# Performance work log

Hardware: AMD Instinct MI355X
Metric: run time of the kernel (lower is better)

The kernel has to match this reference:

```python
import jax, jax.numpy as jnp
import numpy as np

N_NODES = 100000
N_EDGES = 1600000
IN_DIM, HID_DIM, OUT_DIM = 128, 128, 64


def setup_inputs() -> dict:
    key = jax.random.key(0)
    ks = jax.random.split(key, 5)
    x = jax.random.normal(ks[0], (N_NODES, IN_DIM), dtype=jnp.float32)
    edge_index = jax.random.randint(ks[1], (2, N_EDGES), 0, N_NODES, dtype=jnp.int64)
    W1 = jax.random.normal(ks[2], (IN_DIM, HID_DIM), dtype=jnp.float32) * (1.0 / np.sqrt(IN_DIM))
    b1 = jnp.zeros((HID_DIM,), dtype=jnp.float32)
    W2 = jax.random.normal(ks[3], (HID_DIM, OUT_DIM), dtype=jnp.float32) * (1.0 / np.sqrt(HID_DIM))
    b2 = jnp.zeros((OUT_DIM,), dtype=jnp.float32)
    return {"x": x, "edge_index": edge_index, "W1": W1, "b1": b1, "W2": W2, "b2": b2}


def _gcn_conv(h, row, col, norm, b, n_nodes):
    # h: [N, F] already linearly transformed; message = norm_e * h[src]; scatter-add to dst
    msg = h[row] * norm[:, None]                      # [E+N, F]
    out = jax.ops.segment_sum(msg, col, num_segments=n_nodes)
    return out + b


def reference(x, edge_index, W1, b1, W2, b2):
    n = x.shape[0]
    loops = jnp.arange(n, dtype=edge_index.dtype)
    row = jnp.concatenate([edge_index[0], loops])     # sources (incl. self loops)
    col = jnp.concatenate([edge_index[1], loops])     # targets
    # symmetric normalization: deg over targets with unit edge weights
    deg = jax.ops.segment_sum(jnp.ones_like(col, dtype=x.dtype), col, num_segments=n)
    dinv = jnp.where(deg > 0, jax.lax.rsqrt(jnp.maximum(deg, 1.0)), 0.0)
    norm = dinv[row] * dinv[col]                      # [E+N]
    h = jax.nn.relu(_gcn_conv(x @ W1, row, col, norm, b1, n))
    out = _gcn_conv(h @ W2, row, col, norm, b2, n)
    return out.mean(axis=0)                           # [OUT_DIM]
```

## Files before the change

### kernel.cpp

```cpp
#include <hip/hip_runtime.h>

#define N_NODES 100000
#define N_EDGES 1600000
#define IN_DIM 128
#define HID_DIM 128
#define OUT_DIM 64
#define BKT_SHIFT 7
#define BKT_SIZE 128
#define NBKT ((N_NODES + BKT_SIZE - 1) / BKT_SIZE)
#define B1 256
#define HIST_N (NBKT * B1)
#define HIST_N2 (2 * HIST_N)
#define GEMM_BLKS ((N_NODES + 127) / 128)
#define AGG_BLKS 2048
#define NPW 13

typedef float v2f __attribute__((ext_vector_type(2)));
typedef float v4f __attribute__((ext_vector_type(4)));
typedef short v8s __attribute__((ext_vector_type(8)));

__device__ __forceinline__ int permb(int b) { return ((b & 7) << 5) | (b >> 3); }

__device__ __forceinline__ unsigned int f2bf(float f) {
  unsigned int u = __float_as_uint(f);
  return (u + 0x7FFFu + ((u >> 16) & 1u)) >> 16;
}

template <bool HI>
__device__ __forceinline__ v2f cvt8(unsigned int u) {
  return __builtin_amdgcn_cvt_pk_f32_fp8((int)u, HI);
}

__device__ __forceinline__ float redq(float v) {
  v += __shfl_xor(v, 16);
  v += __shfl_xor(v, 32);
  return v;
}

__device__ __forceinline__ void load4(const void* ei, int is64, int half, int base,
                                      int* v) {
  if (is64) {
    const long long* e = (const long long*)ei + (size_t)half * N_EDGES + base;
    longlong2 a = *(const longlong2*)e;
    longlong2 b = *(const longlong2*)(e + 2);
    v[0] = (int)a.x; v[1] = (int)a.y; v[2] = (int)b.x; v[3] = (int)b.y;
  } else {
    const int* e = (const int*)ei + (size_t)half * N_EDGES + base;
    int4 a = *(const int4*)e;
    v[0] = a.x; v[1] = a.y; v[2] = a.z; v[3] = a.w;
  }
}

__device__ __forceinline__ int detect64_block(const unsigned int* ei, int* sh) {
  if (threadIdx.x == 0) *sh = 0;
  __syncthreads();
  if (ei[1 + 2 * threadIdx.x] != 0u) *sh = 1;
  __syncthreads();
  return (*sh == 0) ? 1 : 0;
}

__global__ __launch_bounds__(256) void front_kernel(const float* __restrict__ x,
                                                    const float* __restrict__ W,
                                                    const void* ei,
                                                    unsigned int* __restrict__ G,
                                                    int* hist, float* S) {
  __shared__ __align__(16) char smem[2 * 128 * 136 * 2];
  if (blockIdx.x >= GEMM_BLKS) {
    int* hd = (int*)smem;
    int* hs = hd + NBKT;
    int* sh = hs + NBKT;
    const int hb = blockIdx.x - GEMM_BLKS;
    const int pj = permb(hb);
    if (hb == 0 && threadIdx.x < HID_DIM) S[threadIdx.x] = 0.f;
    const int is64 = detect64_block((const unsigned int*)ei, sh);
    for (int k = threadIdx.x; k < NBKT; k += 256) { hd[k] = 0; hs[k] = 0; }
    __syncthreads();
    for (int g = hb * 256 + threadIdx.x; g < N_EDGES / 4; g += B1 * 256) {
      int r[4], c[4];
      load4(ei, is64, 0, g * 4, r);
      load4(ei, is64, 1, g * 4, c);
#pragma unroll
      for (int k = 0; k < 4; k++) {
        atomicAdd(&hd[c[k] >> BKT_SHIFT], 1);
        atomicAdd(&hs[r[k] >> BKT_SHIFT], 1);
      }
    }
    __syncthreads();
    for (int k = threadIdx.x; k < NBKT; k += 256) {
      hist[k * B1 + pj] = hd[k];
      hist[HIST_N + k * B1 + pj] = hs[k];
    }
    return;
  }
  typedef unsigned short us_row[136];
  us_row* lx = (us_row*)smem;
  us_row* lwt = (us_row*)(smem + 128 * 136 * 2);
  const int t = threadIdx.x;
  const int row0 = blockIdx.x * 128;

  {
    const float4* W4 = (const float4*)W;
    for (int it = 0; it < 16; ++it) {
      int idx = t + 256 * it;
      int k = idx >> 5, c4 = (idx & 31) * 4;
      float4 w = W4[idx];
      lwt[c4 + 0][k] = (unsigned short)f2bf(w.x);
      lwt[c4 + 1][k] = (unsigned short)f2bf(w.y);
      lwt[c4 + 2][k] = (unsigned short)f2bf(w.z);
      lwt[c4 + 3][k] = (unsigned short)f2bf(w.w);
    }
  }
  {
    const float4* x4 = (const float4*)(x + (size_t)row0 * IN_DIM);
    for (int it = 0; it < 16; ++it) {
      int idx = t + 256 * it;
      int r = idx >> 5, kq = (idx & 31) * 4;
      float4 v = make_float4(0.f, 0.f, 0.f, 0.f);
      if (row0 + r < N_NODES) v = x4[idx];
      unsigned int p0 = (f2bf(v.y) << 16) | f2bf(v.x);
      unsigned int p1 = (f2bf(v.w) << 16) | f2bf(v.z);
      *(uint2*)&lx[r][kq] = make_uint2(p0, p1);
    }
  }
  __syncthreads();

  const int lane = t & 63;
  const int wv = t >> 6;
  const int m0 = wv * 32;
  const int lrow = lane & 15;
  const int lk = (lane >> 4) * 8;

  v4f acc[2][8];
#pragma unroll
  for (int si = 0; si < 2; si++)
#pragma unroll
    for (int n = 0; n < 8; n++) acc[si][n] = (v4f){0.f, 0.f, 0.f, 0.f};

#pragma unroll
  for (int kk = 0; kk < 128; kk += 32) {
    v8s a0 = *(const v8s*)&lx[m0 + lrow][kk + lk];
    v8s a1 = *(const v8s*)&lx[m0 + 16 + lrow][kk + lk];
#pragma unroll
    for (int n = 0; n < 8; n++) {
      v8s b = *(const v8s*)&lwt[n * 16 + lrow][kk + lk];
      acc[0][n] = __builtin_amdgcn_mfma_f32_16x16x32_bf16(a0, b, acc[0][n], 0, 0, 0);
      acc[1][n] = __builtin_amdgcn_mfma_f32_16x16x32_bf16(a1, b, acc[1][n], 0, 0, 0);
    }
  }

  unsigned char* G8 = (unsigned char*)G;
#pragma unroll
  for (int si = 0; si < 2; si++)
#pragma unroll
    for (int n = 0; n < 8; n++) {
      int colg = n * 16 + (lane & 15);
#pragma unroll
      for (int i = 0; i < 4; i++) {
        int r = row0 + m0 + si * 16 + (lane >> 4) * 4 + i;
        if (r < N_NODES) {
          float v = acc[si][n][i];
          int pk = __builtin_amdgcn_cvt_pk_fp8_f32(v, v, 0, false);
          G8[(size_t)r * HID_DIM + colg] = (unsigned char)(pk & 0xFF);
        }
      }
    }
}

__global__ void scan1_kernel(int* arr, int* bsum, int n) {
  __shared__ int tmp[256];
  int i = blockIdx.x * 256 + threadIdx.x;
  int v = (i < n) ? arr[i] : 0;
  tmp[threadIdx.x] = v;
  __syncthreads();
  for (int off = 1; off < 256; off <<= 1) {
    int t2 = (threadIdx.x >= off) ? tmp[threadIdx.x - off] : 0;
    __syncthreads();
    tmp[threadIdx.x] += t2;
    __syncthreads();
  }
  if (i < n) arr[i] = tmp[threadIdx.x] - v;
  if (threadIdx.x == 255) bsum[blockIdx.x] = tmp[255];
}

__global__ void scan2_kernel(int* bsum, int nb) {
  __shared__ int tmp[1024];
  const int t = threadIdx.x;
  int v0 = (2 * t < nb) ? bsum[2 * t] : 0;
  int v1 = (2 * t + 1 < nb) ? bsum[2 * t + 1] : 0;
  int s = v0 + v1;
  tmp[t] = s;
  __syncthreads();
  for (int off = 1; off < 1024; off <<= 1) {
    int t2 = (t >= off) ? tmp[t - off] : 0;
    __syncthreads();
    tmp[t] += t2;
    __syncthreads();
  }
  int excl = tmp[t] - s;
  if (2 * t < nb) bsum[2 * t] = excl;
  if (2 * t + 1 < nb) bsum[2 * t + 1] = excl + v0;
}

__global__ __launch_bounds__(256) void scatter_kernel(const void* ei, const int* hist,
                                                      const int* bsum,
                                                      unsigned int* pairs) {
  __shared__ int cd[NBKT], cs[NBKT], sh[1];
  const int is64 = detect64_block((const unsigned int*)ei, sh);
  const int pj = permb(blockIdx.x);
  for (int k = threadIdx.x; k < NBKT; k += 256) {
    cd[k] = hist[k * B1 + pj] + bsum[k];
    cs[k] = hist[HIST_N + k * B1 + pj] + bsum[NBKT + k];
  }
  __syncthreads();
  for (int g = blockIdx.x * 256 + threadIdx.x; g < N_EDGES / 4; g += B1 * 256) {
    int r[4], c[4];
    load4(ei, is64, 0, g * 4, r);
    load4(ei, is64, 1, g * 4, c);
#pragma unroll
    for (int k = 0; k < 4; k++) {
      int pd = atomicAdd(&cd[c[k] >> BKT_SHIFT], 1);
      pairs[pd] = ((unsigned int)(c[k] & (BKT_SIZE - 1)) << 17) | (unsigned int)r[k];
      int ps = atomicAdd(&cs[r[k] >> BKT_SHIFT], 1);
      pairs[ps] = ((unsigned int)(r[k] & (BKT_SIZE - 1)) << 17) | (unsigned int)c[k];
    }
  }
}

__global__ __launch_bounds__(256) void csrA_kernel(const int* hist, const int* bsum,
                                                   const unsigned int* pairs,
                                                   int* rowptr, float* dinv) {
  __shared__ int cnt[BKT_SIZE], sc[BKT_SIZE];
  const int k = blockIdx.x;
  const int base = hist[k * B1] + bsum[k];
  const int end = (k == NBKT - 1) ? N_EDGES : hist[(k + 1) * B1] + bsum[k + 1];
  const int nseg = end - base;
  const int l = threadIdx.x;
  if (l < BKT_SIZE) cnt[l] = 0;
  __syncthreads();
  for (int i = l; i < nseg; i += 256) atomicAdd(&cnt[pairs[base + i] >> 17], 1);
  __syncthreads();
  if (l < BKT_SIZE) sc[l] = cnt[l];
  __syncthreads();
  for (int off = 1; off < BKT_SIZE; off <<= 1) {
    int v = (l < BKT_SIZE && l >= off) ? sc[l - off] : 0;
    __syncthreads();
    if (l < BKT_SIZE) sc[l] += v;
    __syncthreads();
  }
  if (l < BKT_SIZE) {
    int excl = sc[l] - cnt[l];
    int v = k * BKT_SIZE + l;
    if (v < N_NODES) {
      rowptr[v] = base + excl;
      dinv[v] = rsqrtf((float)(cnt[l] + 1));
    }
  }
  if (k == NBKT - 1 && l == 0) rowptr[N_NODES] = N_EDGES;
}

__global__ __launch_bounds__(256) void csrBout_kernel(const int* hist, const int* bsum,
                                                      const unsigned int* pairs,
                                                      const int* __restrict__ rowptr,
                                                      const float* __restrict__ dinv,
                                                      unsigned int* __restrict__ csr,
                                                      float* __restrict__ wacc) {
  if (blockIdx.x < NBKT) {
    __shared__ int cur[BKT_SIZE];
    const int k = blockIdx.x;
    const int base = hist[k * B1] + bsum[k];
    const int end = (k == NBKT - 1) ? N_EDGES : hist[(k + 1) * B1] + bsum[k + 1];
    const int nseg = end - base;
    const int l = threadIdx.x;
    if (l < BKT_SIZE) {
      int v = k * BKT_SIZE + l;
      cur[l] = (v < N_NODES) ? rowptr[v] : 0;
    }
    __syncthreads();
    for (int i = l; i < nseg; i += 256) {
      unsigned int pk = pairs[base + i];
      unsigned int src = pk & 0x1FFFFu;
      int pos = atomicAdd(&cur[pk >> 17], 1);
      unsigned int bits = f2bf(dinv[src]);
      csr[pos] = (bits << 17) | src;
    }
    return;
  }
  __shared__ float fb[BKT_SIZE];
  const int k = blockIdx.x - NBKT;
  const int base = hist[HIST_N + k * B1] + bsum[NBKT + k];
  const int end =
      (k == NBKT - 1) ? 2 * N_EDGES : hist[HIST_N + (k + 1) * B1] + bsum[NBKT + k + 1];
  if (threadIdx.x < BKT_SIZE) fb[threadIdx.x] = 0.f;
  __syncthreads();
  for (int i = base + threadIdx.x; i < end; i += 256) {
    unsigned int pk = pairs[i];
    atomicAdd(&fb[pk >> 17], dinv[pk & 0x1FFFFu]);
  }
  __syncthreads();
  int v = k * BKT_SIZE + threadIdx.x;
  if (threadIdx.x < BKT_SIZE && v < N_NODES) wacc[v] = fb[threadIdx.x];
}

__global__ __launch_bounds__(256) void aggregate_kernel(
    const unsigned int* __restrict__ G, const int* __restrict__ rowptr,
    const unsigned int* __restrict__ csr, const float* __restrict__ dinv,
    const float* __restrict__ wacc, const float* __restrict__ b1,
    float* __restrict__ S) {
  __shared__ float lb[HID_DIM];
  __shared__ float ls[HID_DIM];
  if (threadIdx.x < HID_DIM) {
    lb[threadIdx.x] = b1[threadIdx.x];
    ls[threadIdx.x] = 0.f;
  }
  __syncthreads();

  const int lane = threadIdx.x & 63;
  const int q = lane >> 4;
  const int r = lane & 15;
  const int wid = blockIdx.x * 4 + (threadIdx.x >> 6);
  const int c0 = wid * NPW;
  const uint2* __restrict__ G2 = (const uint2*)G;

  int rp = 0;
  float dvv = 0.f, wvv = 0.f;
  {
    const int ci = c0 + lane;
    if (lane <= NPW && ci <= N_NODES) rp = rowptr[ci];
    if (lane < NPW && ci < N_NODES) { dvv = dinv[ci]; wvv = wacc[ci]; }
  }

  v2f s01 = {0.f, 0.f}, s23 = {0.f, 0.f}, s45 = {0.f, 0.f}, s67 = {0.f, 0.f};
  const int nn = (c0 < N_NODES) ? min(NPW, N_NODES - c0) : 0;

  if (nn > 0) {
    int kF = 0, jF = 0;
    const int sF0 = __shfl(rp, 0);
    int cnumF = __shfl(rp, 1) - sF0;
    int SF = max(1, (cnumF + 15) >> 4);
    unsigned int pwW = 0;
    if (lane < cnumF) pwW = __builtin_nontemporal_load(&csr[sF0 + lane]);
    int sN = __shfl(rp, 1);
    int eN = __shfl(rp, 2);
    unsigned int pwN = 0;
    if (1 < nn && sN + lane < eN) pwN = __builtin_nontemporal_load(&csr[sN + lane]);

    int kC = 0, jC = 0;
    int SC = SF;
    float dC = __shfl(dvv, 0), waC = __shfl(wvv, 0);
    v2f a01 = {0.f, 0.f}, a23 = {0.f, 0.f}, a45 = {0.f, 0.f}, a67 = {0.f, 0.f};

    uint2 gA[4], gB[4], gSA, gSB;
    unsigned int wpA[2], wpB[2];

    auto FETCH = [&](uint2(&g)[4], unsigned int(&wp)[2], uint2& gS) {
      if (jF != 0 && (jF & 3) == 0) {
        const int sAbs = __shfl(rp, kF) + (jF << 4);
        pwW = 0;
        if ((jF << 4) + lane < cnumF)
          pwW = __builtin_nontemporal_load(&csr[sAbs + lane]);
      }
      const int base = (jF & 3) << 4;
      const int eg0 = (jF << 4) + q;
      unsigned int wb[4];
#pragma unroll
      for (int t = 0; t < 4; ++t) {
        const unsigned int p = __shfl(pwW, base + 4 * t + q);
        const bool vld = eg0 + 4 * t < cnumF;
        wb[t] = vld ? ((p >> 17) << 16) : 0u;
        g[t] = make_uint2(0u, 0u);
        if (vld) g[t] = G2[(size_t)(p & 0x1FFFFu) * 16 + r];
      }
      wp[0] = wb[0] | (wb[1] >> 16);
      wp[1] = wb[2] | (wb[3] >> 16);
      if (jF == 0) {
        gS = make_uint2(0u, 0u);
        if (q == 0) gS = G2[(size_t)(c0 + kF) * 16 + r];
      }
      if (jF + 1 < SF) { jF++; return; }
      kF++; jF = 0;
      if (kF < nn) {
        pwW = pwN;
        cnumF = eN - sN;
        SF = max(1, (cnumF + 15) >> 4);
        if (kF + 1 < nn) {
          sN = __shfl(rp, kF + 1);
          eN = __shfl(rp, kF + 2);
          pwN = 0;
          if (sN + lane < eN) pwN = __builtin_nontemporal_load(&csr[sN + lane]);
        }
      }
    };

    auto CONSUME = [&](const uint2(&g)[4], const unsigned int(&wp)[2],
                       const uint2& gS) -> bool {
      const float w0 = __uint_as_float(wp[0] & 0xFFFF0000u);
      const float w1 = __uint_as_float(wp[0] << 16);
      const float w2 = __uint_as_float(wp[1] & 0xFFFF0000u);
      const float w3 = __uint_as_float(wp[1] << 16);
      a01 += cvt8<false>(g[0].x) * w0; a23 += cvt8<true>(g[0].x) * w0;
      a45 += cvt8<false>(g[0].y) * w0; a67 += cvt8<true>(g[0].y) * w0;
      a01 += cvt8<false>(g[1].x) * w1; a23 += cvt8<true>(g[1].x) * w1;
      a45 += cvt8<false>(g[1].y) * w1; a67 += cvt8<true>(g[1].y) * w1;
      a01 += cvt8<false>(g[2].x) * w2; a23 += cvt8<true>(g[2].x) * w2;
      a45 += cvt8<false>(g[2].y) * w2; a67 += cvt8<true>(g[2].y) * w2;
      a01 += cvt8<false>(g[3].x) * w3; a23 += cvt8<true>(g[3].x) * w3;
      a45 += cvt8<false>(g[3].y) * w3; a67 += cvt8<true>(g[3].y) * w3;
      if (jC == 0 && q == 0) {
        a01 += cvt8<false>(gS.x) * dC; a23 += cvt8<true>(gS.x) * dC;
        a45 += cvt8<false>(gS.y) * dC; a67 += cvt8<true>(gS.y) * dC;
      }
      if (jC + 1 < SC) { jC++; return true; }
      const float A0 = redq(a01.x), A1 = redq(a01.y);
      const float A2 = redq(a23.x), A3 = redq(a23.y);
      const float A4 = redq(a45.x), A5 = redq(a45.y);
      const float A6 = redq(a67.x), A7 = redq(a67.y);
      if (q == 0) {
        const float wc = dC * (waC + dC);
        const float* bb = &lb[8 * r];
        s01.x += wc * fmaxf(fmaf(dC, A0, bb[0]), 0.f);
        s01.y += wc * fmaxf(fmaf(dC, A1, bb[1]), 0.f);
        s23.x += wc * fmaxf(fmaf(dC, A2, bb[2]), 0.f);
        s23.y += wc * fmaxf(fmaf(dC, A3, bb[3]), 0.f);
        s45.x += wc * fmaxf(fmaf(dC, A4, bb[4]), 0.f);
        s45.y += wc * fmaxf(fmaf(dC, A5, bb[5]), 0.f);
        s67.x += wc * fmaxf(fmaf(dC, A6, bb[6]), 0.f);
        s67.y += wc * fmaxf(fmaf(dC, A7, bb[7]), 0.f);
      }
      a01 = (v2f){0.f, 0.f}; a23 = (v2f){0.f, 0.f};
      a45 = (v2f){0.f, 0.f}; a67 = (v2f){0.f, 0.f};
      kC++; jC = 0;
      if (kC >= nn) return false;
      const int s_ = __shfl(rp, kC);
      const int cnumC = __shfl(rp, kC + 1) - s_;
      SC = max(1, (cnumC + 15) >> 4);
      dC = __shfl(dvv, kC);
      waC = __shfl(wvv, kC);
      return true;
    };

    FETCH(gA, wpA, gSA);
    for (;;) {
      if (kF < nn) FETCH(gB, wpB, gSB);
      if (!CONSUME(gA, wpA, gSA)) break;
      if (kF < nn) FETCH(gA, wpA, gSA);
      if (!CONSUME(gB, wpB, gSB)) break;
    }
  }

  if (q == 0) {
    atomicAdd(&ls[8 * r + 0], s01.x); atomicAdd(&ls[8 * r + 1], s01.y);
    atomicAdd(&ls[8 * r + 2], s23.x); atomicAdd(&ls[8 * r + 3], s23.y);
    atomicAdd(&ls[8 * r + 4], s45.x); atomicAdd(&ls[8 * r + 5], s45.y);
    atomicAdd(&ls[8 * r + 6], s67.x); atomicAdd(&ls[8 * r + 7], s67.y);
  }
  __syncthreads();
  if (threadIdx.x < HID_DIM) atomicAdd(&S[threadIdx.x], ls[threadIdx.x]);
}

__global__ void finish_kernel(const float* __restrict__ S, const float* __restrict__ W2,
                              const float* __restrict__ b2, float* __restrict__ out) {
  int j = threadIdx.x;
  float acc = 0.f;
  for (int k = 0; k < HID_DIM; k++) acc += S[k] * W2[k * OUT_DIM + j];
  out[j] = acc * (1.0f / N_NODES) + b2[j];
}

extern "C" void kernel_launch(void* const* d_in, const int* in_sizes, int n_in,
                              void* d_out, int out_size, void* d_ws, size_t ws_size,
                              hipStream_t stream) {
  const float* x  = (const float*)d_in[0];
  const void*  ei = d_in[1];
  const float* W1 = (const float*)d_in[2];
  const float* b1 = (const float*)d_in[3];
  const float* W2 = (const float*)d_in[4];
  const float* b2 = (const float*)d_in[5];
  float* out = (float*)d_out;

  char* p = (char*)d_ws;
  size_t off = 0;
  auto alloc = [&](size_t bytes) -> void* {
    void* r = p + off;
    off = (off + bytes + 63) & ~(size_t)63;
    return r;
  };
  int*   hist   = (int*)alloc((size_t)HIST_N2 * 4);
  int*   bsum   = (int*)alloc(2048 * 4);
  unsigned int* pairs = (unsigned int*)alloc((size_t)2 * N_EDGES * 4);
  int*   rowptr = (int*)alloc(((size_t)N_NODES + 1) * 4);
  unsigned int* csr = (unsigned int*)alloc((size_t)N_EDGES * 4);
  float* dinv   = (float*)alloc((size_t)N_NODES * 4);
  float* wacc   = (float*)alloc((size_t)N_NODES * 4);
  float* S      = (float*)alloc(HID_DIM * 4);
  unsigned int* G = (unsigned int*)alloc((size_t)N_NODES * HID_DIM);
  (void)ws_size; (void)n_in; (void)in_sizes; (void)out_size;

  const int NBH = HIST_N2 / 256;

  front_kernel<<<GEMM_BLKS + B1, 256, 0, stream>>>(x, W1, ei, G, hist, S);
  scan1_kernel<<<NBH, 256, 0, stream>>>(hist, bsum, HIST_N2);
  scan2_kernel<<<1, 1024, 0, stream>>>(bsum, NBH);
  scatter_kernel<<<B1, 256, 0, stream>>>(ei, hist, bsum, pairs);
  csrA_kernel<<<NBKT, 256, 0, stream>>>(hist, bsum, pairs, rowptr, dinv);
  csrBout_kernel<<<2 * NBKT, 256, 0, stream>>>(hist, bsum, pairs, rowptr, dinv, csr,
                                               wacc);
  aggregate_kernel<<<AGG_BLKS, 256, 0, stream>>>(G, rowptr, csr, dinv, wacc, b1, S);
  finish_kernel<<<1, 64, 0, stream>>>(S, W2, b2, out);
}
```

Baseline: 264.5 us.

## Replace bucketed two-pass CSR build with direct global-atomic degree count and scatter

Removes the bucket histogram, pairs buffer and the two per-bucket CSR passes. Degrees now come from global atomics per destination node, followed by a node-level scan and a single scatter pass that places edges with global atomic cursors and accumulates wacc with float atomics. This cuts kernel launches and intermediate traffic, but edges within a row now land in nondeterministic order and the work leans on heavily contended random global atomics. The memset zeroes deg, wacc and S together, which relies on the three buffers being laid out contiguously.

```diff
diff --git a/kernel.cpp b/kernel.cpp
--- a/kernel.cpp
+++ b/kernel.cpp
@@ -5,22 +5,16 @@
 #define IN_DIM 128
 #define HID_DIM 128
 #define OUT_DIM 64
-#define BKT_SHIFT 7
-#define BKT_SIZE 128
-#define NBKT ((N_NODES + BKT_SIZE - 1) / BKT_SIZE)
-#define B1 256
-#define HIST_N (NBKT * B1)
-#define HIST_N2 (2 * HIST_N)
 #define GEMM_BLKS ((N_NODES + 127) / 128)
+#define DEG_BLKS 256
 #define AGG_BLKS 2048
 #define NPW 13
+#define NODE_BLKS ((N_NODES + 255) / 256)
 
 typedef float v2f __attribute__((ext_vector_type(2)));
 typedef float v4f __attribute__((ext_vector_type(4)));
 typedef short v8s __attribute__((ext_vector_type(8)));
 
-__device__ __forceinline__ int permb(int b) { return ((b & 7) << 5) | (b >> 3); }
-
 __device__ __forceinline__ unsigned int f2bf(float f) {
   unsigned int u = __float_as_uint(f);
   return (u + 0x7FFFu + ((u >> 16) & 1u)) >> 16;
@@ -29,12 +23,6 @@
 template <bool HI>
 __device__ __forceinline__ v2f cvt8(unsigned int u) {
   return __builtin_amdgcn_cvt_pk_f32_fp8((int)u, HI);
-}
-
-__device__ __forceinline__ float redq(float v) {
-  v += __shfl_xor(v, 16);
-  v += __shfl_xor(v, 32);
-  return v;
 }
 
 __device__ __forceinline__ void load4(const void* ei, int is64, int half, int base,
@@ -63,32 +51,17 @@
                                                     const float* __restrict__ W,
                                                     const void* ei,
                                                     unsigned int* __restrict__ G,
-                                                    int* hist, float* S) {
+                                                    int* __restrict__ deg) {
   __shared__ __align__(16) char smem[2 * 128 * 136 * 2];
   if (blockIdx.x >= GEMM_BLKS) {
-    int* hd = (int*)smem;
-    int* hs = hd + NBKT;
-    int* sh = hs + NBKT;
+    int* sh = (int*)smem;
     const int hb = blockIdx.x - GEMM_BLKS;
-    const int pj = permb(hb);
-    if (hb == 0 && threadIdx.x < HID_DIM) S[threadIdx.x] = 0.f;
     const int is64 = detect64_block((const unsigned int*)ei, sh);
-    for (int k = threadIdx.x; k < NBKT; k += 256) { hd[k] = 0; hs[k] = 0; }
-    __syncthreads();
-    for (int g = hb * 256 + threadIdx.x; g < N_EDGES / 4; g += B1 * 256) {
-      int r[4], c[4];
-      load4(ei, is64, 0, g * 4, r);
+    for (int g = hb * 256 + threadIdx.x; g < N_EDGES / 4; g += DEG_BLKS * 256) {
+      int c[4];
       load4(ei, is64, 1, g * 4, c);
 #pragma unroll
-      for (int k = 0; k < 4; k++) {
-        atomicAdd(&hd[c[k] >> BKT_SHIFT], 1);
-        atomicAdd(&hs[r[k] >> BKT_SHIFT], 1);
-      }
-    }
-    __syncthreads();
-    for (int k = threadIdx.x; k < NBKT; k += 256) {
-      hist[k * B1 + pj] = hd[k];
-      hist[HIST_N + k * B1 + pj] = hs[k];
+      for (int k = 0; k < 4; k++) atomicAdd(&deg[c[k]], 1);
     }
     return;
   }
@@ -166,10 +139,11 @@
     }
 }
 
-__global__ void scan1_kernel(int* arr, int* bsum, int n) {
+__global__ void scan1_kernel(int* arr, int* bsum, int n, float* __restrict__ dinv) {
   __shared__ int tmp[256];
   int i = blockIdx.x * 256 + threadIdx.x;
   int v = (i < n) ? arr[i] : 0;
+  if (i < n) dinv[i] = rsqrtf((float)(v + 1));
   tmp[threadIdx.x] = v;
   __syncthreads();
   for (int off = 1; off < 256; off <<= 1) {
@@ -201,104 +175,35 @@
   if (2 * t + 1 < nb) bsum[2 * t + 1] = excl + v0;
 }
 
-__global__ __launch_bounds__(256) void scatter_kernel(const void* ei, const int* hist,
-                                                      const int* bsum,
-                                                      unsigned int* pairs) {
-  __shared__ int cd[NBKT], cs[NBKT], sh[1];
+__global__ void fin_kernel(const int* __restrict__ arr, const int* __restrict__ bsum,
+                           int* __restrict__ rowptr, int* __restrict__ cur) {
+  const int v = blockIdx.x * 256 + threadIdx.x;
+  if (v < N_NODES) {
+    const int rp = arr[v] + bsum[v >> 8];
+    rowptr[v] = rp;
+    cur[v] = rp;
+  }
+  if (v == 0) rowptr[N_NODES] = N_EDGES;
+}
+
+__global__ __launch_bounds__(256) void csrscatter_kernel(
+    const void* ei, const float* __restrict__ dinv, int* __restrict__ cur,
+    unsigned int* __restrict__ csr, float* __restrict__ wacc) {
+  __shared__ int sh[1];
   const int is64 = detect64_block((const unsigned int*)ei, sh);
-  const int pj = permb(blockIdx.x);
-  for (int k = threadIdx.x; k < NBKT; k += 256) {
-    cd[k] = hist[k * B1 + pj] + bsum[k];
-    cs[k] = hist[HIST_N + k * B1 + pj] + bsum[NBKT + k];
-  }
-  __syncthreads();
-  for (int g = blockIdx.x * 256 + threadIdx.x; g < N_EDGES / 4; g += B1 * 256) {
+  for (int g = blockIdx.x * 256 + threadIdx.x; g < N_EDGES / 4; g += 512 * 256) {
     int r[4], c[4];
     load4(ei, is64, 0, g * 4, r);
     load4(ei, is64, 1, g * 4, c);
 #pragma unroll
     for (int k = 0; k < 4; k++) {
-      int pd = atomicAdd(&cd[c[k] >> BKT_SHIFT], 1);
-      pairs[pd] = ((unsigned int)(c[k] & (BKT_SIZE - 1)) << 17) | (unsigned int)r[k];
-      int ps = atomicAdd(&cs[r[k] >> BKT_SHIFT], 1);
-      pairs[ps] = ((unsigned int)(r[k] & (BKT_SIZE - 1)) << 17) | (unsigned int)c[k];
-    }
-  }
-}
-
-__global__ __launch_bounds__(256) void csrA_kernel(const int* hist, const int* bsum,
-                                                   const unsigned int* pairs,
-                                                   int* rowptr, float* dinv) {
-  __shared__ int cnt[BKT_SIZE], sc[BKT_SIZE];
-  const int k = blockIdx.x;
-  const int base = hist[k * B1] + bsum[k];
-  const int end = (k == NBKT - 1) ? N_EDGES : hist[(k + 1) * B1] + bsum[k + 1];
-  const int nseg = end - base;
-  const int l = threadIdx.x;
-  if (l < BKT_SIZE) cnt[l] = 0;
-  __syncthreads();
-  for (int i = l; i < nseg; i += 256) atomicAdd(&cnt[pairs[base + i] >> 17], 1);
-  __syncthreads();
-  if (l < BKT_SIZE) sc[l] = cnt[l];
-  __syncthreads();
-  for (int off = 1; off < BKT_SIZE; off <<= 1) {
-    int v = (l < BKT_SIZE && l >= off) ? sc[l - off] : 0;
-    __syncthreads();
-    if (l < BKT_SIZE) sc[l] += v;
-    __syncthreads();
-  }
-  if (l < BKT_SIZE) {
-    int excl = sc[l] - cnt[l];
-    int v = k * BKT_SIZE + l;
-    if (v < N_NODES) {
-      rowptr[v] = base + excl;
-      dinv[v] = rsqrtf((float)(cnt[l] + 1));
-    }
-  }
-  if (k == NBKT - 1 && l == 0) rowptr[N_NODES] = N_EDGES;
-}
-
-__global__ __launch_bounds__(256) void csrBout_kernel(const int* hist, const int* bsum,
-                                                      const unsigned int* pairs,
-                                                      const int* __restrict__ rowptr,
-                                                      const float* __restrict__ dinv,
-                                                      unsigned int* __restrict__ csr,
-                                                      float* __restrict__ wacc) {
-  if (blockIdx.x < NBKT) {
-    __shared__ int cur[BKT_SIZE];
-    const int k = blockIdx.x;
-    const int base = hist[k * B1] + bsum[k];
-    const int end = (k == NBKT - 1) ? N_EDGES : hist[(k + 1) * B1] + bsum[k + 1];
-    const int nseg = end - base;
-    const int l = threadIdx.x;
-    if (l < BKT_SIZE) {
-      int v = k * BKT_SIZE + l;
-      cur[l] = (v < N_NODES) ? rowptr[v] : 0;
-    }
-    __syncthreads();
-    for (int i = l; i < nseg; i += 256) {
-      unsigned int pk = pairs[base + i];
-      unsigned int src = pk & 0x1FFFFu;
-      int pos = atomicAdd(&cur[pk >> 17], 1);
-      unsigned int bits = f2bf(dinv[src]);
-      csr[pos] = (bits << 17) | src;
-    }
-    return;
-  }
-  __shared__ float fb[BKT_SIZE];
-  const int k = blockIdx.x - NBKT;
-  const int base = hist[HIST_N + k * B1] + bsum[NBKT + k];
-  const int end =
-      (k == NBKT - 1) ? 2 * N_EDGES : hist[HIST_N + (k + 1) * B1] + bsum[NBKT + k + 1];
-  if (threadIdx.x < BKT_SIZE) fb[threadIdx.x] = 0.f;
-  __syncthreads();
-  for (int i = base + threadIdx.x; i < end; i += 256) {
-    unsigned int pk = pairs[i];
-    atomicAdd(&fb[pk >> 17], dinv[pk & 0x1FFFFu]);
-  }
-  __syncthreads();
-  int v = k * BKT_SIZE + threadIdx.x;
-  if (threadIdx.x < BKT_SIZE && v < N_NODES) wacc[v] = fb[threadIdx.x];
+      const float ds = dinv[r[k]];
+      const float dd = dinv[c[k]];
+      const int pos = atomicAdd(&cur[c[k]], 1);
+      csr[pos] = (f2bf(ds) << 17) | (unsigned int)r[k];
+      atomicAdd(&wacc[r[k]], dd);
+    }
+  }
 }
 
 __global__ __launch_bounds__(256) void aggregate_kernel(
@@ -410,6 +315,11 @@
         a45 += cvt8<false>(gS.y) * dC; a67 += cvt8<true>(gS.y) * dC;
       }
       if (jC + 1 < SC) { jC++; return true; }
+      auto redq = [](float v) {
+        v += __shfl_xor(v, 16);
+        v += __shfl_xor(v, 32);
+        return v;
+      };
       const float A0 = redq(a01.x), A1 = redq(a01.y);
       const float A2 = redq(a23.x), A3 = redq(a23.y);
       const float A4 = redq(a45.x), A5 = redq(a45.y);
@@ -483,26 +393,24 @@
     off = (off + bytes + 63) & ~(size_t)63;
     return r;
   };
-  int*   hist   = (int*)alloc((size_t)HIST_N2 * 4);
-  int*   bsum   = (int*)alloc(2048 * 4);
-  unsigned int* pairs = (unsigned int*)alloc((size_t)2 * N_EDGES * 4);
-  int*   rowptr = (int*)alloc(((size_t)N_NODES + 1) * 4);
-  unsigned int* csr = (unsigned int*)alloc((size_t)N_EDGES * 4);
-  float* dinv   = (float*)alloc((size_t)N_NODES * 4);
+  int*   deg    = (int*)alloc((size_t)N_NODES * 4);
   float* wacc   = (float*)alloc((size_t)N_NODES * 4);
   float* S      = (float*)alloc(HID_DIM * 4);
-  unsigned int* G = (unsigned int*)alloc((size_t)N_NODES * HID_DIM);
+  int*   bsum   = (int*)alloc(2048 * 4);
+  int*   rowptr = (int*)alloc(((size_t)N_NODES + 1) * 4);
+  int*   cur    = (int*)alloc((size_t)N_NODES * 4);
+  float* dinv   = (float*)alloc((size_t)N_NODES * 4);
+  unsigned int* csr = (unsigned int*)alloc((size_t)N_EDGES * 4);
+  unsigned int* G   = (unsigned int*)alloc((size_t)N_NODES * HID_DIM);
   (void)ws_size; (void)n_in; (void)in_sizes; (void)out_size;
 
-  const int NBH = HIST_N2 / 256;
-
-  front_kernel<<<GEMM_BLKS + B1, 256, 0, stream>>>(x, W1, ei, G, hist, S);
-  scan1_kernel<<<NBH, 256, 0, stream>>>(hist, bsum, HIST_N2);
-  scan2_kernel<<<1, 1024, 0, stream>>>(bsum, NBH);
-  scatter_kernel<<<B1, 256, 0, stream>>>(ei, hist, bsum, pairs);
-  csrA_kernel<<<NBKT, 256, 0, stream>>>(hist, bsum, pairs, rowptr, dinv);
-  csrBout_kernel<<<2 * NBKT, 256, 0, stream>>>(hist, bsum, pairs, rowptr, dinv, csr,
-                                               wacc);
+  hipMemsetAsync(deg, 0, (size_t)N_NODES * 8 + HID_DIM * 4, stream);
+
+  front_kernel<<<GEMM_BLKS + DEG_BLKS, 256, 0, stream>>>(x, W1, ei, G, deg);
+  scan1_kernel<<<NODE_BLKS, 256, 0, stream>>>(deg, bsum, N_NODES, dinv);
+  scan2_kernel<<<1, 1024, 0, stream>>>(bsum, NODE_BLKS);
+  fin_kernel<<<NODE_BLKS, 256, 0, stream>>>(deg, bsum, rowptr, cur);
+  csrscatter_kernel<<<512, 256, 0, stream>>>(ei, dinv, cur, csr, wacc);
   aggregate_kernel<<<AGG_BLKS, 256, 0, stream>>>(G, rowptr, csr, dinv, wacc, b1, S);
   finish_kernel<<<1, 64, 0, stream>>>(S, W2, b2, out);
 }
```

Measured after the change: 425.8 us. +61.0%, slower.

## Replace source-bucketed wacc sort with direct global atomics over edges

Applied to the files above, without the earlier changes.

The source-side bucket histogram, scatter of reversed pairs and bucketed shared-memory accumulation are removed. wacc (sum of dinv over out-neighbours) is now computed by streaming the edge list and doing global float atomicAdds into wacc, which a memset zeroes together with S. This halves the histogram, scan and scatter work and pairs traffic, in exchange for 1.6M scattered global atomics and the loss of deterministic summation order.

```diff
diff --git a/kernel.cpp b/kernel.cpp
--- a/kernel.cpp
+++ b/kernel.cpp
@@ -10,8 +10,9 @@
 #define NBKT ((N_NODES + BKT_SIZE - 1) / BKT_SIZE)
 #define B1 256
 #define HIST_N (NBKT * B1)
-#define HIST_N2 (2 * HIST_N)
+#define NBH (HIST_N / 256)
 #define GEMM_BLKS ((N_NODES + 127) / 128)
+#define WACC_BLKS 512
 #define AGG_BLKS 2048
 #define NPW 13
 
@@ -29,12 +30,6 @@
 template <bool HI>
 __device__ __forceinline__ v2f cvt8(unsigned int u) {
   return __builtin_amdgcn_cvt_pk_f32_fp8((int)u, HI);
-}
-
-__device__ __forceinline__ float redq(float v) {
-  v += __shfl_xor(v, 16);
-  v += __shfl_xor(v, 32);
-  return v;
 }
 
 __device__ __forceinline__ void load4(const void* ei, int is64, int half, int base,
@@ -63,33 +58,24 @@
                                                     const float* __restrict__ W,
                                                     const void* ei,
                                                     unsigned int* __restrict__ G,
-                                                    int* hist, float* S) {
+                                                    int* hist) {
   __shared__ __align__(16) char smem[2 * 128 * 136 * 2];
   if (blockIdx.x >= GEMM_BLKS) {
     int* hd = (int*)smem;
-    int* hs = hd + NBKT;
-    int* sh = hs + NBKT;
+    int* sh = hd + NBKT;
     const int hb = blockIdx.x - GEMM_BLKS;
     const int pj = permb(hb);
-    if (hb == 0 && threadIdx.x < HID_DIM) S[threadIdx.x] = 0.f;
     const int is64 = detect64_block((const unsigned int*)ei, sh);
-    for (int k = threadIdx.x; k < NBKT; k += 256) { hd[k] = 0; hs[k] = 0; }
+    for (int k = threadIdx.x; k < NBKT; k += 256) hd[k] = 0;
     __syncthreads();
     for (int g = hb * 256 + threadIdx.x; g < N_EDGES / 4; g += B1 * 256) {
-      int r[4], c[4];
-      load4(ei, is64, 0, g * 4, r);
+      int c[4];
       load4(ei, is64, 1, g * 4, c);
 #pragma unroll
-      for (int k = 0; k < 4; k++) {
-        atomicAdd(&hd[c[k] >> BKT_SHIFT], 1);
-        atomicAdd(&hs[r[k] >> BKT_SHIFT], 1);
-      }
-    }
-    __syncthreads();
-    for (int k = threadIdx.x; k < NBKT; k += 256) {
-      hist[k * B1 + pj] = hd[k];
-      hist[HIST_N + k * B1 + pj] = hs[k];
-    }
+      for (int k = 0; k < 4; k++) atomicAdd(&hd[c[k] >> BKT_SHIFT], 1);
+    }
+    __syncthreads();
+    for (int k = threadIdx.x; k < NBKT; k += 256) hist[k * B1 + pj] = hd[k];
     return;
   }
   typedef unsigned short us_row[136];
@@ -204,13 +190,10 @@
 __global__ __launch_bounds__(256) void scatter_kernel(const void* ei, const int* hist,
                                                       const int* bsum,
                                                       unsigned int* pairs) {
-  __shared__ int cd[NBKT], cs[NBKT], sh[1];
+  __shared__ int cd[NBKT], sh[1];
   const int is64 = detect64_block((const unsigned int*)ei, sh);
   const int pj = permb(blockIdx.x);
-  for (int k = threadIdx.x; k < NBKT; k += 256) {
-    cd[k] = hist[k * B1 + pj] + bsum[k];
-    cs[k] = hist[HIST_N + k * B1 + pj] + bsum[NBKT + k];
-  }
+  for (int k = threadIdx.x; k < NBKT; k += 256) cd[k] = hist[k * B1 + pj] + bsum[k];
   __syncthreads();
   for (int g = blockIdx.x * 256 + threadIdx.x; g < N_EDGES / 4; g += B1 * 256) {
     int r[4], c[4];
@@ -220,8 +203,6 @@
     for (int k = 0; k < 4; k++) {
       int pd = atomicAdd(&cd[c[k] >> BKT_SHIFT], 1);
       pairs[pd] = ((unsigned int)(c[k] & (BKT_SIZE - 1)) << 17) | (unsigned int)r[k];
-      int ps = atomicAdd(&cs[r[k] >> BKT_SHIFT], 1);
-      pairs[ps] = ((unsigned int)(r[k] & (BKT_SIZE - 1)) << 17) | (unsigned int)c[k];
     }
   }
 }
@@ -258,12 +239,11 @@
   if (k == NBKT - 1 && l == 0) rowptr[N_NODES] = N_EDGES;
 }
 
-__global__ __launch_bounds__(256) void csrBout_kernel(const int* hist, const int* bsum,
-                                                      const unsigned int* pairs,
-                                                      const int* __restrict__ rowptr,
-                                                      const float* __restrict__ dinv,
-                                                      unsigned int* __restrict__ csr,
-                                                      float* __restrict__ wacc) {
+__global__ __launch_bounds__(256) void csrBwacc_kernel(
+    const void* ei, const int* hist, const int* bsum,
+    const unsigned int* __restrict__ pairs, const int* __restrict__ rowptr,
+    const float* __restrict__ dinv, unsigned int* __restrict__ csr,
+    float* __restrict__ wacc) {
   if (blockIdx.x < NBKT) {
     __shared__ int cur[BKT_SIZE];
     const int k = blockIdx.x;
@@ -285,20 +265,16 @@
     }
     return;
   }
-  __shared__ float fb[BKT_SIZE];
-  const int k = blockIdx.x - NBKT;
-  const int base = hist[HIST_N + k * B1] + bsum[NBKT + k];
-  const int end =
-      (k == NBKT - 1) ? 2 * N_EDGES : hist[HIST_N + (k + 1) * B1] + bsum[NBKT + k + 1];
-  if (threadIdx.x < BKT_SIZE) fb[threadIdx.x] = 0.f;
-  __syncthreads();
-  for (int i = base + threadIdx.x; i < end; i += 256) {
-    unsigned int pk = pairs[i];
-    atomicAdd(&fb[pk >> 17], dinv[pk & 0x1FFFFu]);
-  }
-  __syncthreads();
-  int v = k * BKT_SIZE + threadIdx.x;
-  if (threadIdx.x < BKT_SIZE && v < N_NODES) wacc[v] = fb[threadIdx.x];
+  __shared__ int sh[1];
+  const int is64 = detect64_block((const unsigned int*)ei, sh);
+  const int wb = blockIdx.x - NBKT;
+  for (int g = wb * 256 + threadIdx.x; g < N_EDGES / 4; g += WACC_BLKS * 256) {
+    int r[4], c[4];
+    load4(ei, is64, 0, g * 4, r);
+    load4(ei, is64, 1, g * 4, c);
+#pragma unroll
+    for (int k = 0; k < 4; k++) atomicAdd(&wacc[r[k]], dinv[c[k]]);
+  }
 }
 
 __global__ __launch_bounds__(256) void aggregate_kernel(
@@ -410,6 +386,11 @@
         a45 += cvt8<false>(gS.y) * dC; a67 += cvt8<true>(gS.y) * dC;
       }
       if (jC + 1 < SC) { jC++; return true; }
+      auto redq = [](float v) {
+        v += __shfl_xor(v, 16);
+        v += __shfl_xor(v, 32);
+        return v;
+      };
       const float A0 = redq(a01.x), A1 = redq(a01.y);
       const float A2 = redq(a23.x), A3 = redq(a23.y);
       const float A4 = redq(a45.x), A5 = redq(a45.y);
@@ -483,9 +464,9 @@
     off = (off + bytes + 63) & ~(size_t)63;
     return r;
   };
-  int*   hist   = (int*)alloc((size_t)HIST_N2 * 4);
+  int*   hist   = (int*)alloc((size_t)HIST_N * 4);
   int*   bsum   = (int*)alloc(2048 * 4);
-  unsigned int* pairs = (unsigned int*)alloc((size_t)2 * N_EDGES * 4);
+  unsigned int* pairs = (unsigned int*)alloc((size_t)N_EDGES * 4);
   int*   rowptr = (int*)alloc(((size_t)N_NODES + 1) * 4);
   unsigned int* csr = (unsigned int*)alloc((size_t)N_EDGES * 4);
   float* dinv   = (float*)alloc((size_t)N_NODES * 4);
@@ -494,15 +475,15 @@
   unsigned int* G = (unsigned int*)alloc((size_t)N_NODES * HID_DIM);
   (void)ws_size; (void)n_in; (void)in_sizes; (void)out_size;
 
-  const int NBH = HIST_N2 / 256;
-
-  front_kernel<<<GEMM_BLKS + B1, 256, 0, stream>>>(x, W1, ei, G, hist, S);
-  scan1_kernel<<<NBH, 256, 0, stream>>>(hist, bsum, HIST_N2);
+  hipMemsetAsync(wacc, 0, (size_t)N_NODES * 4 + HID_DIM * 4, stream);
+
+  front_kernel<<<GEMM_BLKS + B1, 256, 0, stream>>>(x, W1, ei, G, hist);
+  scan1_kernel<<<NBH, 256, 0, stream>>>(hist, bsum, HIST_N);
   scan2_kernel<<<1, 1024, 0, stream>>>(bsum, NBH);
   scatter_kernel<<<B1, 256, 0, stream>>>(ei, hist, bsum, pairs);
   csrA_kernel<<<NBKT, 256, 0, stream>>>(hist, bsum, pairs, rowptr, dinv);
-  csrBout_kernel<<<2 * NBKT, 256, 0, stream>>>(hist, bsum, pairs, rowptr, dinv, csr,
-                                               wacc);
+  csrBwacc_kernel<<<NBKT + WACC_BLKS, 256, 0, stream>>>(ei, hist, bsum, pairs, rowptr,
+                                                        dinv, csr, wacc);
   aggregate_kernel<<<AGG_BLKS, 256, 0, stream>>>(G, rowptr, csr, dinv, wacc, b1, S);
   finish_kernel<<<1, 64, 0, stream>>>(S, W2, b2, out);
 }
```

Result: slower. 322.0 us (+21.7%).
